# Performance work log

Measured on AMD Instinct MI355X. Metric: run time of the kernel, lower is better.

The kernel has to match this reference:

```python
import jax, jax.numpy as jnp
import numpy as np

INPUT_DIM = 128
HIDDEN_DIM = 256
TOP_K = 512
M = 8192
N = 8192


def setup_inputs() -> dict:
    key = jax.random.key(0)
    ks = jax.random.split(key, 10)
    s_in = 1.0 / np.sqrt(INPUT_DIM)
    s_h = 1.0 / np.sqrt(HIDDEN_DIM)
    return {
        "desc0": jax.random.normal(ks[0], (1, M, INPUT_DIM), jnp.float32),
        "desc1": jax.random.normal(ks[1], (1, N, INPUT_DIM), jnp.float32),
        # mlpc0: Linear(in,h) -> ReLU -> Linear(h,h); weights stored [in,out]
        "W0a": jax.random.uniform(ks[2], (INPUT_DIM, HIDDEN_DIM), jnp.float32, -s_in, s_in),
        "b0a": jax.random.uniform(ks[3], (HIDDEN_DIM,), jnp.float32, -s_in, s_in),
        "W0b": jax.random.uniform(ks[4], (HIDDEN_DIM, HIDDEN_DIM), jnp.float32, -s_h, s_h),
        "b0b": jax.random.uniform(ks[5], (HIDDEN_DIM,), jnp.float32, -s_h, s_h),
        "W1a": jax.random.uniform(ks[6], (INPUT_DIM, HIDDEN_DIM), jnp.float32, -s_in, s_in),
        "b1a": jax.random.uniform(ks[7], (HIDDEN_DIM,), jnp.float32, -s_in, s_in),
        "W1b": jax.random.uniform(ks[8], (HIDDEN_DIM, HIDDEN_DIM), jnp.float32, -s_h, s_h),
        "b1b": jax.random.uniform(ks[9], (HIDDEN_DIM,), jnp.float32, -s_h, s_h),
    }


def _mlp(x, Wa, ba, Wb, bb):
    h = jax.nn.relu(x @ Wa + ba)
    return h @ Wb + bb


def reference(desc0, desc1, W0a, b0a, W0b, b0b, W1a, b1a, W1b, b1b):
    mdesc0 = _mlp(desc0, W0a, b0a, W0b, b0b)  # [1, M, H]
    mdesc1 = _mlp(desc1, W1a, b1a, W1b, b1b)  # [1, N, H]
    sim = jnp.einsum("bmd,bnd->bmn", mdesc0, mdesc1)  # [1, M, N]
    flat = sim[0].reshape(-1)
    _, top_idx = jax.lax.top_k(flat, TOP_K)
    n = sim.shape[2]
    rows = top_idx // n
    cols = top_idx % n
    top_k_indices_2d = jnp.stack([rows, cols], axis=1)  # [TOP_K, 2]
    return top_k_indices_2d, sim
```

## Files before the change

### kernel.cpp

```cpp
#include <hip/hip_runtime.h>
#include <stdint.h>

#define H_DIM 256
#define NCOL 8192
#define TOPK 512
#define CAND_CAP 8192

typedef unsigned short u16;
typedef __attribute__((ext_vector_type(8))) __bf16 bf16x8;
typedef __attribute__((ext_vector_type(4))) float f32x4;
typedef unsigned __attribute__((address_space(3))) lds_u32;
typedef const unsigned __attribute__((address_space(1))) glb_u32;

__device__ __forceinline__ unsigned fkey(float f) {
  unsigned u = __float_as_uint(f);
  unsigned m = (unsigned)((int)u >> 31) | 0x80000000u;
  return u ^ m;
}

__device__ __forceinline__ u16 f2bf_rne(float f) {
  unsigned u = __float_as_uint(f);
  return (u16)((u + 0x7fffu + ((u >> 16) & 1u)) >> 16);
}

__device__ __forceinline__ float bf2f(u16 h) {
  return __uint_as_float(((unsigned)h) << 16);
}

__global__ __launch_bounds__(256) void mlp_fused(
    const float* __restrict__ X0, const float* __restrict__ W0a,
    const float* __restrict__ b0a, const float* __restrict__ W0b,
    const float* __restrict__ b0b, float* __restrict__ Y0,
    u16* __restrict__ h0, u16* __restrict__ l0,
    const float* __restrict__ X1, const float* __restrict__ W1a,
    const float* __restrict__ b1a, const float* __restrict__ W1b,
    const float* __restrict__ b1b, float* __restrict__ Y1,
    u16* __restrict__ h1, u16* __restrict__ l1,
    unsigned* __restrict__ ghist, unsigned* __restrict__ counter,
    unsigned* __restrict__ nwork) {
  __shared__ float Xs[16 * 128];
  __shared__ float Hs[16 * 256];
  const int t = threadIdx.x;
  if (blockIdx.x == 0) {
    for (int i = t; i < 4096; i += 256) ghist[i] = 0;
    if (t == 0) { *counter = 0; *nwork = 0; }
  }
  const int half = blockIdx.x >> 9;
  const float* X = half ? X1 : X0;
  const float* Wa = half ? W1a : W0a;
  const float* ba = half ? b1a : b0a;
  const float* Wb = half ? W1b : W0b;
  const float* bb_ = half ? b1b : b0b;
  float* Y = half ? Y1 : Y0;
  u16* hi = half ? h1 : h0;
  u16* lo = half ? l1 : l0;
  const int row0 = (blockIdx.x & 511) * 16;

  for (int f = t; f < 512; f += 256) {
    *(float4*)(Xs + f * 4) = *(const float4*)(X + (size_t)row0 * 128 + f * 4);
  }
  __syncthreads();
  const int cg = (t & 63) * 4;
  const int rg = (t >> 6) * 4;

  {
    float acc[4][4];
#pragma unroll
    for (int r = 0; r < 4; r++)
#pragma unroll
      for (int c = 0; c < 4; c++) acc[r][c] = 0.f;
    for (int d = 0; d < 128; d += 4) {
      float4 w0 = *(const float4*)(Wa + (d + 0) * H_DIM + cg);
      float4 w1 = *(const float4*)(Wa + (d + 1) * H_DIM + cg);
      float4 w2 = *(const float4*)(Wa + (d + 2) * H_DIM + cg);
      float4 w3 = *(const float4*)(Wa + (d + 3) * H_DIM + cg);
#pragma unroll
      for (int r = 0; r < 4; r++) {
        float4 x = *(const float4*)(Xs + (rg + r) * 128 + d);
#pragma unroll
        for (int c = 0; c < 4; c++) {
          float a = acc[r][c];
          a = fmaf(x.x, ((const float*)&w0)[c], a);
          a = fmaf(x.y, ((const float*)&w1)[c], a);
          a = fmaf(x.z, ((const float*)&w2)[c], a);
          a = fmaf(x.w, ((const float*)&w3)[c], a);
          acc[r][c] = a;
        }
      }
    }
    const float4 bv = *(const float4*)(ba + cg);
#pragma unroll
    for (int r = 0; r < 4; r++) {
      float4 v;
      v.x = fmaxf(acc[r][0] + bv.x, 0.f);
      v.y = fmaxf(acc[r][1] + bv.y, 0.f);
      v.z = fmaxf(acc[r][2] + bv.z, 0.f);
      v.w = fmaxf(acc[r][3] + bv.w, 0.f);
      *(float4*)(Hs + (rg + r) * 256 + cg) = v;
    }
  }
  __syncthreads();

  {
    float acc[4][4];
#pragma unroll
    for (int r = 0; r < 4; r++)
#pragma unroll
      for (int c = 0; c < 4; c++) acc[r][c] = 0.f;
    for (int d = 0; d < 256; d += 4) {
      float4 w0 = *(const float4*)(Wb + (d + 0) * H_DIM + cg);
      float4 w1 = *(const float4*)(Wb + (d + 1) * H_DIM + cg);
      float4 w2 = *(const float4*)(Wb + (d + 2) * H_DIM + cg);
      float4 w3 = *(const float4*)(Wb + (d + 3) * H_DIM + cg);
#pragma unroll
      for (int r = 0; r < 4; r++) {
        float4 x = *(const float4*)(Hs + (rg + r) * 256 + d);
#pragma unroll
        for (int c = 0; c < 4; c++) {
          float a = acc[r][c];
          a = fmaf(x.x, ((const float*)&w0)[c], a);
          a = fmaf(x.y, ((const float*)&w1)[c], a);
          a = fmaf(x.z, ((const float*)&w2)[c], a);
          a = fmaf(x.w, ((const float*)&w3)[c], a);
          acc[r][c] = a;
        }
      }
    }
    const float4 bv = *(const float4*)(bb_ + cg);
#pragma unroll
    for (int r = 0; r < 4; r++) {
      float4 v;
      v.x = acc[r][0] + bv.x;
      v.y = acc[r][1] + bv.y;
      v.z = acc[r][2] + bv.z;
      v.w = acc[r][3] + bv.w;
      const size_t grow = (size_t)(row0 + rg + r);
      *(float4*)(Y + grow * H_DIM + cg) = v;
      ushort4 hv, lv;
      hv.x = f2bf_rne(v.x); lv.x = f2bf_rne(v.x - bf2f(hv.x));
      hv.y = f2bf_rne(v.y); lv.y = f2bf_rne(v.y - bf2f(hv.y));
      hv.z = f2bf_rne(v.z); lv.z = f2bf_rne(v.z - bf2f(hv.z));
      hv.w = f2bf_rne(v.w); lv.w = f2bf_rne(v.w - bf2f(hv.w));
      *(ushort4*)(hi + grow * H_DIM + cg) = hv;
      *(ushort4*)(lo + grow * H_DIM + cg) = lv;
    }
  }
}

__global__ __launch_bounds__(512, 2) void gemm_sim_mfma(const u16* __restrict__ Ah,
                                                        const u16* __restrict__ Al,
                                                        const u16* __restrict__ Bh,
                                                        const u16* __restrict__ Bl,
                                                        float* __restrict__ C,
                                                        unsigned* __restrict__ ghist,
                                                        unsigned* __restrict__ tilemax) {
  __shared__ __align__(16) char SB[131072];
  const int t = threadIdx.x;
  const int wave = t >> 6, lane = t & 63;
  const int wm = wave >> 2, wn = wave & 3;
  const int bid = blockIdx.x;
  const int swz = (bid & 7) * 128 + (bid >> 3);
  const int m0 = (swz >> 5) * 256, n0 = (swz & 31) * 256;

  f32x4 acc[8][4];
#pragma unroll
  for (int i = 0; i < 8; i++)
#pragma unroll
    for (int j = 0; j < 4; j++) acc[i][j] = (f32x4){0.f, 0.f, 0.f, 0.f};

  const int srow8 = t >> 3;
  const int sA = (t & 7) ^ (srow8 & 7);
  const u16* pAsrc = (sA < 4) ? Ah : Al;
  const u16* pBsrc = (sA < 4) ? Bh : Bl;
  const int scolE = (sA & 3) * 8;
  const int lrow = lane & 15;
  const int kq16 = (lane >> 4) << 4;
  const int asz = (lrow & 7) << 4;
  const int cH = kq16 ^ asz;
  const int cL = (64 + kq16) ^ asz;

  auto STAGE = [&](int bsel, int tt) {
    const int kofs = tt * 32;
    char* base = SB + bsel * 65536;
    const size_t ar = (size_t)(m0 + srow8) * H_DIM + kofs + scolE;
    const size_t br = (size_t)(n0 + srow8) * H_DIM + kofs + scolE;
#pragma unroll
    for (int i = 0; i < 4; i++)
      __builtin_amdgcn_global_load_lds((glb_u32*)(pAsrc + ar + (size_t)i * 64 * H_DIM),
                                       (lds_u32*)(base + i * 8192 + wave * 1024), 16, 0, 0);
#pragma unroll
    for (int i = 0; i < 4; i++)
      __builtin_amdgcn_global_load_lds((glb_u32*)(pBsrc + br + (size_t)i * 64 * H_DIM),
                                       (lds_u32*)(base + 32768 + i * 8192 + wave * 1024), 16, 0, 0);
  };

  STAGE(0, 0);
  for (int tt = 0; tt < 8; ++tt) {
    if (tt < 7) {
      STAGE((tt + 1) & 1, tt + 1);
      asm volatile("s_waitcnt vmcnt(8)" ::: "memory");
    } else {
      asm volatile("s_waitcnt vmcnt(0)" ::: "memory");
    }
    __builtin_amdgcn_s_barrier();
    asm volatile("" ::: "memory");
    const char* bb = SB + (tt & 1) * 65536;
    const char* bA = bb + (wm * 128 + lrow) * 128;
    const char* bB = bb + 32768 + (wn * 64 + lrow) * 128;

    bf16x8 aH[8], bH[4];
#pragma unroll
    for (int fm = 0; fm < 8; fm++) aH[fm] = *(const bf16x8*)(bA + fm * 2048 + cH);
#pragma unroll
    for (int fn = 0; fn < 4; fn++) bH[fn] = *(const bf16x8*)(bB + fn * 2048 + cH);
    __builtin_amdgcn_s_setprio(1);
#pragma unroll
    for (int fm = 0; fm < 8; fm++)
#pragma unroll
      for (int fn = 0; fn < 4; fn++)
        acc[fm][fn] = __builtin_amdgcn_mfma_f32_16x16x32_bf16(aH[fm], bH[fn], acc[fm][fn], 0, 0, 0);
    __builtin_amdgcn_s_setprio(0);
    __builtin_amdgcn_s_barrier();

    {
      bf16x8 bL[4];
#pragma unroll
      for (int fn = 0; fn < 4; fn++) bL[fn] = *(const bf16x8*)(bB + fn * 2048 + cL);
      __builtin_amdgcn_s_setprio(1);
#pragma unroll
      for (int fm = 0; fm < 8; fm++)
#pragma unroll
        for (int fn = 0; fn < 4; fn++)
          acc[fm][fn] = __builtin_amdgcn_mfma_f32_16x16x32_bf16(aH[fm], bL[fn], acc[fm][fn], 0, 0, 0);
      __builtin_amdgcn_s_setprio(0);
    }
    __builtin_amdgcn_s_barrier();

    {
      bf16x8 aL[8];
#pragma unroll
      for (int fm = 0; fm < 8; fm++) aL[fm] = *(const bf16x8*)(bA + fm * 2048 + cL);
      __builtin_amdgcn_s_setprio(1);
#pragma unroll
      for (int fm = 0; fm < 8; fm++)
#pragma unroll
        for (int fn = 0; fn < 4; fn++)
          acc[fm][fn] = __builtin_amdgcn_mfma_f32_16x16x32_bf16(aL[fm], bH[fn], acc[fm][fn], 0, 0, 0);
      __builtin_amdgcn_s_setprio(0);
    }
    __builtin_amdgcn_s_barrier();
    asm volatile("" ::: "memory");
  }

  {
    float mx0 = -3.4e38f, mx1 = -3.4e38f;
#pragma unroll
    for (int fm = 0; fm < 4; fm++)
#pragma unroll
      for (int fn = 0; fn < 4; fn++)
#pragma unroll
        for (int q = 0; q < 4; q++) {
          mx0 = fmaxf(mx0, acc[fm][fn][q]);
          mx1 = fmaxf(mx1, acc[fm + 4][fn][q]);
        }
#pragma unroll
    for (int off = 1; off < 64; off <<= 1) {
      mx0 = fmaxf(mx0, __shfl_xor(mx0, off, 64));
      mx1 = fmaxf(mx1, __shfl_xor(mx1, off, 64));
    }
    if (lane == 0) {
      const int str = (m0 >> 6) + wm * 2, stc = (n0 >> 6) + wn;
      tilemax[str * 128 + stc] = fkey(mx0);
      tilemax[(str + 1) * 128 + stc] = fkey(mx1);
    }
  }

  unsigned* hist = (unsigned*)SB;
  float* Ct = (float*)(SB + 16384);
  for (int i = t; i < 4096; i += 512) hist[i] = 0;
  __syncthreads();
#pragma unroll
  for (int ch = 0; ch < 4; ++ch) {
    if (wm == (ch >> 1)) {
      const int fmb = (ch & 1) * 4;
#pragma unroll
      for (int fi = 0; fi < 4; fi++)
#pragma unroll
        for (int fn = 0; fn < 4; fn++)
#pragma unroll
          for (int q = 0; q < 4; q++)
            Ct[(fi * 16 + (lane >> 4) * 4 + q) * 260 + wn * 64 + fn * 16 + lrow] =
                acc[fmb + fi][fn][q];
    }
    __syncthreads();
#pragma unroll
    for (int u = 0; u < 8; ++u) {
      const int idx = t + u * 512;
      const int row = idx >> 6, c4 = idx & 63;
      float4 v = *(const float4*)(Ct + row * 260 + c4 * 4);
      *(float4*)(C + (size_t)(m0 + ch * 64 + row) * NCOL + n0 + c4 * 4) = v;
      atomicAdd(&hist[fkey(v.x) >> 20], 1u);
      atomicAdd(&hist[fkey(v.y) >> 20], 1u);
      atomicAdd(&hist[fkey(v.z) >> 20], 1u);
      atomicAdd(&hist[fkey(v.w) >> 20], 1u);
    }
    __syncthreads();
  }
  for (int bq = t; bq < 4096; bq += 512) {
    unsigned cc = hist[bq];
    if (cc) atomicAdd(&ghist[bq], cc);
  }
}

__global__ __launch_bounds__(256) void collect_scan(const unsigned* __restrict__ ghist,
                                                    const unsigned* __restrict__ tilemax,
                                                    unsigned* __restrict__ thrm_out,
                                                    int* __restrict__ worklist,
                                                    unsigned* __restrict__ nwork) {
  __shared__ unsigned part[256];
  __shared__ unsigned thr_sh;
  const int t = threadIdx.x;
  unsigned s = 0;
#pragma unroll
  for (int b = 0; b < 16; b++) s += ghist[t * 16 + b];
  part[t] = s;
  __syncthreads();
  for (int off = 1; off < 256; off <<= 1) {
    unsigned v = part[t] + ((t + off < 256) ? part[t + off] : 0u);
    __syncthreads();
    part[t] = v;
    __syncthreads();
  }
  if (part[t] >= TOPK && (t == 255 || part[t + 1] < TOPK)) {
    unsigned cum = (t == 255) ? 0u : part[t + 1];
    int bsel = t * 16;
    for (int b = t * 16 + 15; b >= t * 16; --b) {
      cum += ghist[b];
      if (cum >= TOPK) { bsel = b; break; }
    }
    thr_sh = (unsigned)bsel << 20;
  }
  __syncthreads();
  const unsigned thr = thr_sh;
  const unsigned thr_m = thr > 4096u ? thr - 4096u : 0u;
  if (t == 0) *thrm_out = thr_m;
  for (int i = t; i < 16384; i += 256) {
    if (tilemax[i] >= thr_m) {
      unsigned p = atomicAdd(nwork, 1u);
      worklist[p] = i;
    }
  }
}

__device__ __forceinline__ void cand_push(unsigned kapprox, unsigned thr_m, unsigned idx,
                                          const float* __restrict__ m0f,
                                          const float* __restrict__ m1f,
                                          unsigned long long* __restrict__ cand,
                                          unsigned* __restrict__ counter) {
  if (kapprox >= thr_m) {
    const unsigned row = idx >> 13;
    const unsigned col = idx & 8191u;
    const float4* a4 = (const float4*)(m0f + (size_t)row * H_DIM);
    const float4* b4 = (const float4*)(m1f + (size_t)col * H_DIM);
    float v = 0.f;
#pragma unroll 8
    for (int k = 0; k < H_DIM / 4; k++) {
      float4 a = a4[k], b = b4[k];
      v = fmaf(a.x, b.x, v);
      v = fmaf(a.y, b.y, v);
      v = fmaf(a.z, b.z, v);
      v = fmaf(a.w, b.w, v);
    }
    unsigned p = atomicAdd(counter, 1u);
    if (p < CAND_CAP)
      cand[p] = ((unsigned long long)fkey(v) << 32) |
                (unsigned long long)(0xFFFFFFFFu - idx);
  }
}

__global__ __launch_bounds__(256) void collect_gather(const float* __restrict__ sim,
                                                      const unsigned* __restrict__ thrm_p,
                                                      const int* __restrict__ worklist,
                                                      const unsigned* __restrict__ nwork,
                                                      const float* __restrict__ m0f,
                                                      const float* __restrict__ m1f,
                                                      unsigned long long* __restrict__ cand,
                                                      unsigned* __restrict__ counter) {
  const unsigned thr_m = *thrm_p;
  const int nw = (int)*nwork;
  const int t = threadIdx.x;
  for (int w = blockIdx.x; w < nw; w += gridDim.x) {
    const int sid = worklist[w];
    const int r0 = (sid >> 7) << 6, c0 = (sid & 127) << 6;
    const float4* base = (const float4*)(sim + (size_t)r0 * NCOL + c0);
#pragma unroll
    for (int u = 0; u < 4; ++u) {
      const int f = t + u * 256;
      const int row = f >> 4, q4 = f & 15;
      float4 v = base[(size_t)row * (NCOL / 4) + q4];
      const unsigned gidx = (unsigned)(r0 + row) * NCOL + c0 + q4 * 4;
      cand_push(fkey(v.x), thr_m, gidx + 0u, m0f, m1f, cand, counter);
      cand_push(fkey(v.y), thr_m, gidx + 1u, m0f, m1f, cand, counter);
      cand_push(fkey(v.z), thr_m, gidx + 2u, m0f, m1f, cand, counter);
      cand_push(fkey(v.w), thr_m, gidx + 3u, m0f, m1f, cand, counter);
    }
  }
}

__global__ __launch_bounds__(1024) void sort_topk(const unsigned long long* __restrict__ cand,
                                                  const unsigned* __restrict__ counter,
                                                  float* __restrict__ out) {
  __shared__ unsigned long long top[TOPK];
  __shared__ unsigned wred[16];
  __shared__ unsigned long long pfx_sh;
  __shared__ unsigned cnt_sh;
  const int t = threadIdx.x;
  const int n = (int)min(*counter, (unsigned)CAND_CAP);
  unsigned long long e[CAND_CAP / 1024];
#pragma unroll
  for (int u = 0; u < CAND_CAP / 1024; ++u) {
    const int i = t + u * 1024;
    e[u] = (i < n) ? cand[i] : 0ULL;
  }
  if (t == 0) cnt_sh = 0;
  __syncthreads();
  unsigned long long pfx = 0;
  for (int b = 63; b >= 0; --b) {
    const unsigned long long q = pfx | (1ULL << b);
    unsigned c = 0;
#pragma unroll
    for (int u = 0; u < CAND_CAP / 1024; ++u) c += (e[u] >= q) ? 1u : 0u;
#pragma unroll
    for (int off = 32; off; off >>= 1) c += __shfl_down(c, off, 64);
    if ((t & 63) == 0) wred[t >> 6] = c;
    __syncthreads();
    if (t == 0) {
      unsigned tot = 0;
#pragma unroll
      for (int w = 0; w < 16; ++w) tot += wred[w];
      pfx_sh = (tot >= TOPK) ? q : pfx;
    }
    __syncthreads();
    pfx = pfx_sh;
  }
#pragma unroll
  for (int u = 0; u < CAND_CAP / 1024; ++u) {
    if (e[u] >= pfx) {
      unsigned p = atomicAdd(&cnt_sh, 1u);
      if (p < TOPK) top[p] = e[u];
    }
  }
  __syncthreads();
  for (int k = 2; k <= TOPK; k <<= 1) {
    for (int j = k >> 1; j > 0; j >>= 1) {
      if (t < TOPK) {
        const int l = t ^ j;
        if (l > t) {
          const bool desc = ((t & k) == 0);
          unsigned long long a = top[t], b2 = top[l];
          if (desc ? (a < b2) : (a > b2)) { top[t] = b2; top[l] = a; }
        }
      }
      __syncthreads();
    }
  }
  if (t < TOPK) {
    const unsigned idx = 0xFFFFFFFFu - (unsigned)(top[t] & 0xFFFFFFFFull);
    out[t * 2 + 0] = (float)(idx >> 13);
    out[t * 2 + 1] = (float)(idx & 8191u);
  }
}

extern "C" void kernel_launch(void* const* d_in, const int* in_sizes, int n_in,
                              void* d_out, int out_size, void* d_ws, size_t ws_size,
                              hipStream_t stream) {
  const float* desc0 = (const float*)d_in[0];
  const float* desc1 = (const float*)d_in[1];
  const float* W0a = (const float*)d_in[2];
  const float* b0a = (const float*)d_in[3];
  const float* W0b = (const float*)d_in[4];
  const float* b0b = (const float*)d_in[5];
  const float* W1a = (const float*)d_in[6];
  const float* b1a = (const float*)d_in[7];
  const float* W1b = (const float*)d_in[8];
  const float* b1b = (const float*)d_in[9];

  char* ws = (char*)d_ws;
  unsigned* ghist = (unsigned*)ws;
  unsigned* counter = (unsigned*)(ws + 16384);
  unsigned* thrm = (unsigned*)(ws + 16388);
  unsigned* nwork = (unsigned*)(ws + 16392);
  unsigned long long* cand = (unsigned long long*)(ws + 16448);
  unsigned* tilemax = (unsigned*)(ws + 98304);
  int* worklist = (int*)(ws + 163840);
  float* mdesc0f = (float*)(ws + 262144);
  float* mdesc1f = mdesc0f + 8192 * 256;
  u16* Ahh = (u16*)(mdesc1f + 8192 * 256);
  u16* All = Ahh + 8192 * 256;
  u16* Bhh = All + 8192 * 256;
  u16* Bll = Bhh + 8192 * 256;

  float* outf = (float*)d_out;
  float* sim = outf + TOPK * 2;

  mlp_fused<<<1024, 256, 0, stream>>>(
      desc0, W0a, b0a, W0b, b0b, mdesc0f, Ahh, All,
      desc1, W1a, b1a, W1b, b1b, mdesc1f, Bhh, Bll, ghist, counter, nwork);

  gemm_sim_mfma<<<1024, 512, 0, stream>>>(Ahh, All, Bhh, Bll, sim, ghist, tilemax);
  collect_scan<<<1, 256, 0, stream>>>(ghist, tilemax, thrm, worklist, nwork);
  collect_gather<<<1024, 256, 0, stream>>>(sim, thrm, worklist, nwork, mdesc0f, mdesc1f,
                                           cand, counter);
  sort_topk<<<1, 1024, 0, stream>>>(cand, counter, outf);
}
```

Measured before the change: 552.6 us.

## Fuse threshold scan into gather, retile GEMM block mapping, merge MFMA phases

Three separate changes. The single-block collect_scan kernel is merged into the gather kernel: every block recomputes the histogram threshold and then scans tilemax directly instead of reading a worklist, which removes one kernel launch and the serial one-block stage. The GEMM block-to-tile mapping now gives each XCD a contiguous band of row tiles, aiming at better L2 reuse. The three MFMA phases per k-step now share one barrier, with the low-part fragments loaded earlier, which cuts barriers but raises register pressure.

```diff
diff --git a/kernel.cpp b/kernel.cpp
--- a/kernel.cpp
+++ b/kernel.cpp
@@ -36,14 +36,13 @@
     const float* __restrict__ b1a, const float* __restrict__ W1b,
     const float* __restrict__ b1b, float* __restrict__ Y1,
     u16* __restrict__ h1, u16* __restrict__ l1,
-    unsigned* __restrict__ ghist, unsigned* __restrict__ counter,
-    unsigned* __restrict__ nwork) {
+    unsigned* __restrict__ ghist, unsigned* __restrict__ counter) {
   __shared__ float Xs[16 * 128];
   __shared__ float Hs[16 * 256];
   const int t = threadIdx.x;
   if (blockIdx.x == 0) {
     for (int i = t; i < 4096; i += 256) ghist[i] = 0;
-    if (t == 0) { *counter = 0; *nwork = 0; }
+    if (t == 0) *counter = 0;
   }
   const int half = blockIdx.x >> 9;
   const float* X = half ? X1 : X0;
@@ -159,14 +158,20 @@
   const int wave = t >> 6, lane = t & 63;
   const int wm = wave >> 2, wn = wave & 3;
   const int bid = blockIdx.x;
-  const int swz = (bid & 7) * 128 + (bid >> 3);
-  const int m0 = (swz >> 5) * 256, n0 = (swz & 31) * 256;
+  const int xcd = bid & 7;
+  const int i = bid >> 3;
+  const int band = i >> 6;
+  const int j = i & 63;
+  const int tcol = j >> 1;
+  const int rr = j & 1;
+  const int trow = xcd * 4 + band * 2 + rr;
+  const int m0 = trow * 256, n0 = tcol * 256;
 
   f32x4 acc[8][4];
 #pragma unroll
-  for (int i = 0; i < 8; i++)
-#pragma unroll
-    for (int j = 0; j < 4; j++) acc[i][j] = (f32x4){0.f, 0.f, 0.f, 0.f};
+  for (int ii = 0; ii < 8; ii++)
+#pragma unroll
+    for (int jj = 0; jj < 4; jj++) acc[ii][jj] = (f32x4){0.f, 0.f, 0.f, 0.f};
 
   const int srow8 = t >> 3;
   const int sA = (t & 7) ^ (srow8 & 7);
@@ -185,13 +190,13 @@
     const size_t ar = (size_t)(m0 + srow8) * H_DIM + kofs + scolE;
     const size_t br = (size_t)(n0 + srow8) * H_DIM + kofs + scolE;
 #pragma unroll
-    for (int i = 0; i < 4; i++)
-      __builtin_amdgcn_global_load_lds((glb_u32*)(pAsrc + ar + (size_t)i * 64 * H_DIM),
-                                       (lds_u32*)(base + i * 8192 + wave * 1024), 16, 0, 0);
-#pragma unroll
-    for (int i = 0; i < 4; i++)
-      __builtin_amdgcn_global_load_lds((glb_u32*)(pBsrc + br + (size_t)i * 64 * H_DIM),
-                                       (lds_u32*)(base + 32768 + i * 8192 + wave * 1024), 16, 0, 0);
+    for (int q = 0; q < 4; q++)
+      __builtin_amdgcn_global_load_lds((glb_u32*)(pAsrc + ar + (size_t)q * 64 * H_DIM),
+                                       (lds_u32*)(base + q * 8192 + wave * 1024), 16, 0, 0);
+#pragma unroll
+    for (int q = 0; q < 4; q++)
+      __builtin_amdgcn_global_load_lds((glb_u32*)(pBsrc + br + (size_t)q * 64 * H_DIM),
+                                       (lds_u32*)(base + 32768 + q * 8192 + wave * 1024), 16, 0, 0);
   };
 
   STAGE(0, 0);
@@ -208,11 +213,13 @@
     const char* bA = bb + (wm * 128 + lrow) * 128;
     const char* bB = bb + 32768 + (wn * 64 + lrow) * 128;
 
-    bf16x8 aH[8], bH[4];
+    bf16x8 aH[8], bH[4], bL[4], aL[8];
 #pragma unroll
     for (int fm = 0; fm < 8; fm++) aH[fm] = *(const bf16x8*)(bA + fm * 2048 + cH);
 #pragma unroll
     for (int fn = 0; fn < 4; fn++) bH[fn] = *(const bf16x8*)(bB + fn * 2048 + cH);
+#pragma unroll
+    for (int fn = 0; fn < 4; fn++) bL[fn] = *(const bf16x8*)(bB + fn * 2048 + cL);
     __builtin_amdgcn_s_setprio(1);
 #pragma unroll
     for (int fm = 0; fm < 8; fm++)
@@ -220,34 +227,20 @@
       for (int fn = 0; fn < 4; fn++)
         acc[fm][fn] = __builtin_amdgcn_mfma_f32_16x16x32_bf16(aH[fm], bH[fn], acc[fm][fn], 0, 0, 0);
     __builtin_amdgcn_s_setprio(0);
-    __builtin_amdgcn_s_barrier();
-
-    {
-      bf16x8 bL[4];
-#pragma unroll
-      for (int fn = 0; fn < 4; fn++) bL[fn] = *(const bf16x8*)(bB + fn * 2048 + cL);
-      __builtin_amdgcn_s_setprio(1);
-#pragma unroll
-      for (int fm = 0; fm < 8; fm++)
-#pragma unroll
-        for (int fn = 0; fn < 4; fn++)
-          acc[fm][fn] = __builtin_amdgcn_mfma_f32_16x16x32_bf16(aH[fm], bL[fn], acc[fm][fn], 0, 0, 0);
-      __builtin_amdgcn_s_setprio(0);
-    }
-    __builtin_amdgcn_s_barrier();
-
-    {
-      bf16x8 aL[8];
-#pragma unroll
-      for (int fm = 0; fm < 8; fm++) aL[fm] = *(const bf16x8*)(bA + fm * 2048 + cL);
-      __builtin_amdgcn_s_setprio(1);
-#pragma unroll
-      for (int fm = 0; fm < 8; fm++)
-#pragma unroll
-        for (int fn = 0; fn < 4; fn++)
-          acc[fm][fn] = __builtin_amdgcn_mfma_f32_16x16x32_bf16(aL[fm], bH[fn], acc[fm][fn], 0, 0, 0);
-      __builtin_amdgcn_s_setprio(0);
-    }
+#pragma unroll
+    for (int fm = 0; fm < 8; fm++) aL[fm] = *(const bf16x8*)(bA + fm * 2048 + cL);
+    __builtin_amdgcn_s_setprio(1);
+#pragma unroll
+    for (int fm = 0; fm < 8; fm++)
+#pragma unroll
+      for (int fn = 0; fn < 4; fn++)
+        acc[fm][fn] = __builtin_amdgcn_mfma_f32_16x16x32_bf16(aH[fm], bL[fn], acc[fm][fn], 0, 0, 0);
+#pragma unroll
+    for (int fm = 0; fm < 8; fm++)
+#pragma unroll
+      for (int fn = 0; fn < 4; fn++)
+        acc[fm][fn] = __builtin_amdgcn_mfma_f32_16x16x32_bf16(aL[fm], bH[fn], acc[fm][fn], 0, 0, 0);
+    __builtin_amdgcn_s_setprio(0);
     __builtin_amdgcn_s_barrier();
     asm volatile("" ::: "memory");
   }
@@ -277,7 +270,7 @@
 
   unsigned* hist = (unsigned*)SB;
   float* Ct = (float*)(SB + 16384);
-  for (int i = t; i < 4096; i += 512) hist[i] = 0;
+  for (int ii = t; ii < 4096; ii += 512) hist[ii] = 0;
   __syncthreads();
 #pragma unroll
   for (int ch = 0; ch < 4; ++ch) {
@@ -309,46 +302,6 @@
   for (int bq = t; bq < 4096; bq += 512) {
     unsigned cc = hist[bq];
     if (cc) atomicAdd(&ghist[bq], cc);
-  }
-}
-
-__global__ __launch_bounds__(256) void collect_scan(const unsigned* __restrict__ ghist,
-                                                    const unsigned* __restrict__ tilemax,
-                                                    unsigned* __restrict__ thrm_out,
-                                                    int* __restrict__ worklist,
-                                                    unsigned* __restrict__ nwork) {
-  __shared__ unsigned part[256];
-  __shared__ unsigned thr_sh;
-  const int t = threadIdx.x;
-  unsigned s = 0;
-#pragma unroll
-  for (int b = 0; b < 16; b++) s += ghist[t * 16 + b];
-  part[t] = s;
-  __syncthreads();
-  for (int off = 1; off < 256; off <<= 1) {
-    unsigned v = part[t] + ((t + off < 256) ? part[t + off] : 0u);
-    __syncthreads();
-    part[t] = v;
-    __syncthreads();
-  }
-  if (part[t] >= TOPK && (t == 255 || part[t + 1] < TOPK)) {
-    unsigned cum = (t == 255) ? 0u : part[t + 1];
-    int bsel = t * 16;
-    for (int b = t * 16 + 15; b >= t * 16; --b) {
-      cum += ghist[b];
-      if (cum >= TOPK) { bsel = b; break; }
-    }
-    thr_sh = (unsigned)bsel << 20;
-  }
-  __syncthreads();
-  const unsigned thr = thr_sh;
-  const unsigned thr_m = thr > 4096u ? thr - 4096u : 0u;
-  if (t == 0) *thrm_out = thr_m;
-  for (int i = t; i < 16384; i += 256) {
-    if (tilemax[i] >= thr_m) {
-      unsigned p = atomicAdd(nwork, 1u);
-      worklist[p] = i;
-    }
   }
 }
 
@@ -378,19 +331,43 @@
   }
 }
 
-__global__ __launch_bounds__(256) void collect_gather(const float* __restrict__ sim,
-                                                      const unsigned* __restrict__ thrm_p,
-                                                      const int* __restrict__ worklist,
-                                                      const unsigned* __restrict__ nwork,
-                                                      const float* __restrict__ m0f,
-                                                      const float* __restrict__ m1f,
-                                                      unsigned long long* __restrict__ cand,
-                                                      unsigned* __restrict__ counter) {
-  const unsigned thr_m = *thrm_p;
-  const int nw = (int)*nwork;
+__global__ __launch_bounds__(256) void collect(const float* __restrict__ sim,
+                                               const unsigned* __restrict__ ghist,
+                                               const unsigned* __restrict__ tilemax,
+                                               const float* __restrict__ m0f,
+                                               const float* __restrict__ m1f,
+                                               unsigned long long* __restrict__ cand,
+                                               unsigned* __restrict__ counter) {
+  __shared__ unsigned part[256];
+  __shared__ unsigned thr_sh;
   const int t = threadIdx.x;
-  for (int w = blockIdx.x; w < nw; w += gridDim.x) {
-    const int sid = worklist[w];
+  {
+    unsigned s = 0;
+#pragma unroll
+    for (int b = 0; b < 16; b++) s += ghist[t * 16 + b];
+    part[t] = s;
+    __syncthreads();
+    for (int off = 1; off < 256; off <<= 1) {
+      unsigned v = part[t] + ((t + off < 256) ? part[t + off] : 0u);
+      __syncthreads();
+      part[t] = v;
+      __syncthreads();
+    }
+    if (part[t] >= TOPK && (t == 255 || part[t + 1] < TOPK)) {
+      unsigned cum = (t == 255) ? 0u : part[t + 1];
+      int bsel = t * 16;
+      for (int b = t * 16 + 15; b >= t * 16; --b) {
+        cum += ghist[b];
+        if (cum >= TOPK) { bsel = b; break; }
+      }
+      thr_sh = (unsigned)bsel << 20;
+    }
+    __syncthreads();
+  }
+  const unsigned thr = thr_sh;
+  const unsigned thr_m = thr > 4096u ? thr - 4096u : 0u;
+  for (int sid = blockIdx.x; sid < 16384; sid += gridDim.x) {
+    if (tilemax[sid] < thr_m) continue;
     const int r0 = (sid >> 7) << 6, c0 = (sid & 127) << 6;
     const float4* base = (const float4*)(sim + (size_t)r0 * NCOL + c0);
 #pragma unroll
@@ -488,11 +465,8 @@
   char* ws = (char*)d_ws;
   unsigned* ghist = (unsigned*)ws;
   unsigned* counter = (unsigned*)(ws + 16384);
-  unsigned* thrm = (unsigned*)(ws + 16388);
-  unsigned* nwork = (unsigned*)(ws + 16392);
   unsigned long long* cand = (unsigned long long*)(ws + 16448);
   unsigned* tilemax = (unsigned*)(ws + 98304);
-  int* worklist = (int*)(ws + 163840);
   float* mdesc0f = (float*)(ws + 262144);
   float* mdesc1f = mdesc0f + 8192 * 256;
   u16* Ahh = (u16*)(mdesc1f + 8192 * 256);
@@ -505,11 +479,9 @@
 
   mlp_fused<<<1024, 256, 0, stream>>>(
       desc0, W0a, b0a, W0b, b0b, mdesc0f, Ahh, All,
-      desc1, W1a, b1a, W1b, b1b, mdesc1f, Bhh, Bll, ghist, counter, nwork);
+      desc1, W1a, b1a, W1b, b1b, mdesc1f, Bhh, Bll, ghist, counter);
 
   gemm_sim_mfma<<<1024, 512, 0, stream>>>(Ahh, All, Bhh, Bll, sim, ghist, tilemax);
-  collect_scan<<<1, 256, 0, stream>>>(ghist, tilemax, thrm, worklist, nwork);
-  collect_gather<<<1024, 256, 0, stream>>>(sim, thrm, worklist, nwork, mdesc0f, mdesc1f,
-                                           cand, counter);
+  collect<<<1024, 256, 0, stream>>>(sim, ghist, tilemax, mdesc0f, mdesc1f, cand, counter);
   sort_topk<<<1, 1024, 0, stream>>>(cand, counter, outf);
 }
```

Measured after the change: 611.7 us. 1.11x slower.
